# Kernel tuning notes

Hardware: AMD Instinct MI355X
Metric: run time of the kernel (lower is better)

The kernel has to match this reference:

```python
import jax, jax.numpy as jnp
import numpy as np
from jax.scipy.linalg import solve_triangular

S = 64            # number of weight samples (Xi.shape[0])
OUT = 256         # out_channels
IN_CH, K = 64, 3
F = IN_CH * K * K # in_features == inducing_batch == 576
LOG_PREC_INIT = -4.0
LOG_PREC_LR = 1.0


def setup_inputs() -> dict:
    key = jax.random.key(0)
    k1, k2, k3, k4 = jax.random.split(key, 4)
    Xi = jax.random.normal(k1, (S, 128, F), jnp.float32)          # only shape[0] is used
    Xi_param = jax.random.normal(k2, (1, F, F), jnp.float32)      # self.Xi: [1, inducing_batch, in_features]
    u = jax.random.normal(k3, (OUT, F, 1), jnp.float32)           # self.u
    log_prec_scaled = (LOG_PREC_INIT / LOG_PREC_LR) * jnp.ones((1, 1, F), jnp.float32)
    Z = jax.random.normal(k4, (S, OUT, F, 1), jnp.float32)        # internal randn noise, made explicit
    return dict(Xi=Xi, Xi_param=Xi_param, u=u, log_prec_scaled=log_prec_scaled, Z=Z)


def reference(Xi, Xi_param, u, log_prec_scaled, Z):
    S_ = Xi.shape[0]
    Fd = Xi_param.shape[-1]
    O = u.shape[0]
    # log_prec = log_prec_lr * log_prec_scaled  (precs == 1)
    log_prec = LOG_PREC_LR * log_prec_scaled[0]                    # [1, F]
    Xe = jnp.broadcast_to(Xi_param, (S_, Fd, Fd))                  # [S, I, F]
    XiLT = jnp.exp(log_prec) * jnp.swapaxes(Xe, -1, -2)            # [S, F, I]  (prec_L is None branch)
    XiLXi = XiLT @ Xe                                              # [S, F, F]
    XiLY = jnp.einsum('sfi,oi->sfo', XiLT, u[..., 0])              # [S, F, O]  (torch: [S, O, F, 1])
    # NealPrior over in_shape: precision = fan_in * I, fan_in = in_features
    prior_prec = float(Fd)
    prec = XiLXi + prior_prec * jnp.eye(Fd, dtype=XiLXi.dtype)     # [S, F, F]
    L = jnp.linalg.cholesky(prec)
    logdet_prec = 2.0 * jnp.sum(jnp.log(jnp.diagonal(L, axis1=-2, axis2=-1)), -1)  # [S]
    logdet_prec_tot = O * logdet_prec                              # expand(S, O).sum(-1)
    # cholesky_solve(XiLY, L): prec^{-1} XiLY, batched over O via RHS columns
    mean = solve_triangular(L, solve_triangular(L, XiLY, lower=True), lower=True, trans=1)  # [S, F, O]
    Zm = jnp.swapaxes(Z[..., 0], -1, -2)                           # [S, F, O]
    dW = solve_triangular(L, Zm, lower=True, trans=1)              # L^T dW = Z
    sample_fo = mean + dW                                          # [S, F, O]
    sample = jnp.swapaxes(sample_fo, -1, -2)                       # [S, O, F] == self._sample
    # logP = mvnormal_log_prob_unnorm(prior_prec, sample^T):  -0.5 tr(x^T P x) + 0.5*O*logdet(P)
    logP = (-0.5 * prior_prec * jnp.sum(sample_fo ** 2, (-1, -2))
            + 0.5 * O * Fd * jnp.log(jnp.asarray(prior_prec, sample.dtype)))
    logQ = -0.5 * jnp.sum(Z ** 2, (-1, -2, -3)) + 0.5 * logdet_prec_tot
    logpq = logP - logQ                                            # [S]
    return sample, logpq
```

## Files before the change

### kernel.cpp

```cpp
#include <hip/hip_runtime.h>

#define F 576
#define OUTC 256
#define SNUM 64
#define PP 576.0f
#define NBLK 36

__device__ __forceinline__ void gbar(int* cnt, int barid) {
  __syncthreads();
  if (threadIdx.x == 0) {
    __builtin_amdgcn_fence(__ATOMIC_RELEASE, "agent");
    __hip_atomic_fetch_add(cnt, 1, __ATOMIC_RELAXED, __HIP_MEMORY_SCOPE_AGENT);
    int target = barid * NBLK;
    while (__hip_atomic_load(cnt, __ATOMIC_RELAXED, __HIP_MEMORY_SCOPE_AGENT) < target) {
      __builtin_amdgcn_s_sleep(2);
    }
    __builtin_amdgcn_fence(__ATOMIC_ACQUIRE, "agent");
  }
  __syncthreads();
}

__device__ __forceinline__ void mm16(const float (*As)[68], const float (*Bs)[68],
                                     float acc[4][4], int tx, int ty) {
#pragma unroll
  for (int k = 0; k < 32; ++k) {
    float4 a4 = *(const float4*)&As[k][ty * 4];
    float4 b4 = *(const float4*)&Bs[k][tx * 4];
    float av[4] = {a4.x, a4.y, a4.z, a4.w};
    float bv[4] = {b4.x, b4.y, b4.z, b4.w};
#pragma unroll
    for (int r = 0; r < 4; ++r)
#pragma unroll
      for (int c = 0; c < 4; ++c) acc[r][c] += av[r] * bv[c];
  }
}

__device__ void tile_gemm(const float* __restrict__ A, int lda,
                          const float* __restrict__ B, int ldb,
                          float* __restrict__ C, int ldc,
                          int m0, int n0, int K, float sgn,
                          float (*As)[68], float (*Bs)[68]) {
  int t = threadIdx.x, tx = t & 15, ty = t >> 4;
  float acc[4][4] = {};
  for (int k0 = 0; k0 < K; k0 += 32) {
    int rr = t >> 2, kq = t & 3;
    const float* ap = &A[(m0 + rr) * lda + k0 + kq * 8];
    float4 a0 = *(const float4*)ap;
    float4 a1 = *(const float4*)(ap + 4);
    As[kq*8+0][rr] = a0.x; As[kq*8+1][rr] = a0.y;
    As[kq*8+2][rr] = a0.z; As[kq*8+3][rr] = a0.w;
    As[kq*8+4][rr] = a1.x; As[kq*8+5][rr] = a1.y;
    As[kq*8+6][rr] = a1.z; As[kq*8+7][rr] = a1.w;
    int col = t & 63, kr = t >> 6;
#pragma unroll
    for (int kk = 0; kk < 32; kk += 4)
      Bs[kr + kk][col] = B[(k0 + kr + kk) * ldb + n0 + col];
    __syncthreads();
    mm16(As, Bs, acc, tx, ty);
    __syncthreads();
  }
#pragma unroll
  for (int r = 0; r < 4; ++r)
#pragma unroll
    for (int c = 0; c < 4; ++c)
      C[(m0 + ty*4 + r) * ldc + n0 + tx*4 + c] = sgn * acc[r][c];
}

__device__ void diag_factor(float* Ts ) {
  int t = threadIdx.x;
  __syncthreads();
  if (t < 64) {
    int l = t;
    float r[64];
#pragma unroll
    for (int g = 0; g < 64; ++g) r[g] = Ts[l*66 + g];
#pragma unroll
    for (int j = 0; j < 64; ++j) {
      float d = __shfl(r[j], j, 64);
      float inv = 1.0f / sqrtf(d);
      float c = r[j] * inv;
      r[j] = c;
#pragma unroll
      for (int g = j + 1; g < 64; ++g)
        r[g] = fmaf(-__shfl(c, g, 64), c, r[g]);
    }
#pragma unroll
    for (int g = 0; g < 64; ++g) Ts[l*66 + g] = r[g];
  }
  __syncthreads();
}

__device__ void panel_phase(float* __restrict__ G, int k0, int b,
                            float* Ts, float* invd) {
  int t = threadIdx.x;
  for (int idx = t; idx < 64 * 64; idx += 256) {
    int i = idx >> 6, j = idx & 63;
    Ts[i*66 + j] = G[(k0 + i) * F + k0 + j];
  }
  __syncthreads();
  if (t < 64) invd[t] = 1.0f / Ts[t*66 + t];
  __syncthreads();
  int l = t & 63, w = t >> 6;
  int r0 = k0 + 64 + b * 16 + w * 4;
  float v0 = G[(r0 + 0) * F + k0 + l];
  float v1 = G[(r0 + 1) * F + k0 + l];
  float v2 = G[(r0 + 2) * F + k0 + l];
  float v3 = G[(r0 + 3) * F + k0 + l];
#pragma unroll
  for (int j = 0; j < 64; ++j) {
    float dj = invd[j];
    float x0 = __shfl(v0, j, 64) * dj;
    float x1 = __shfl(v1, j, 64) * dj;
    float x2 = __shfl(v2, j, 64) * dj;
    float x3 = __shfl(v3, j, 64) * dj;
    if (l > j) {
      float lj = Ts[l*66 + j];
      v0 = fmaf(-x0, lj, v0);
      v1 = fmaf(-x1, lj, v1);
      v2 = fmaf(-x2, lj, v2);
      v3 = fmaf(-x3, lj, v3);
    }
  }
  float dl = invd[l];
  G[(r0 + 0) * F + k0 + l] = v0 * dl;
  G[(r0 + 1) * F + k0 + l] = v1 * dl;
  G[(r0 + 2) * F + k0 + l] = v2 * dl;
  G[(r0 + 3) * F + k0 + l] = v3 * dl;
}

__device__ void upd_phase(float* __restrict__ G, int k0, int ti, int tj, bool fuse,
                          float (*As)[68], float (*Bs)[68], float* Ts) {
  int b0 = k0 + 64;
  int i0 = b0 + ti * 64, j0 = b0 + tj * 64;
  int t = threadIdx.x, tx = t & 15, ty = t >> 4;
  float acc[4][4] = {};
  for (int kk0 = 0; kk0 < 64; kk0 += 32) {
    for (int idx = t; idx < 64 * 32; idx += 256) {
      int ii = idx >> 5, kk = idx & 31;
      As[kk][ii] = G[(i0 + ii) * F + k0 + kk0 + kk];
      Bs[kk][ii] = G[(j0 + ii) * F + k0 + kk0 + kk];
    }
    __syncthreads();
#pragma unroll
    for (int k = 0; k < 32; ++k) {
      float a[4], b[4];
#pragma unroll
      for (int m = 0; m < 4; ++m) { a[m] = As[k][ty*4 + m]; b[m] = Bs[k][tx*4 + m]; }
#pragma unroll
      for (int r = 0; r < 4; ++r)
#pragma unroll
        for (int c = 0; c < 4; ++c) acc[r][c] += a[r] * b[c];
    }
    __syncthreads();
  }
  if (!fuse) {
#pragma unroll
    for (int r = 0; r < 4; ++r)
#pragma unroll
      for (int c = 0; c < 4; ++c)
        G[(i0 + ty*4 + r) * F + j0 + tx*4 + c] -= acc[r][c];
  } else {
#pragma unroll
    for (int r = 0; r < 4; ++r)
#pragma unroll
      for (int c = 0; c < 4; ++c)
        Ts[(ty*4 + r)*66 + tx*4 + c] =
            G[(i0 + ty*4 + r) * F + j0 + tx*4 + c] - acc[r][c];
    diag_factor(Ts);
    for (int idx = t; idx < 64 * 64; idx += 256) {
      int i = idx >> 6, j = idx & 63;
      if (j <= i) G[(i0 + i) * F + j0 + j] = Ts[i*66 + j];
    }
  }
}

__device__ void base_inv_phase(const float* __restrict__ G, float* __restrict__ LI,
                               int blk, float* Ts, float* invd) {
  int base = blk * 64, t = threadIdx.x;
  for (int idx = t; idx < 64 * 64; idx += 256) {
    int i = idx >> 6, j = idx & 63;
    Ts[i*66 + j] = G[(base + i) * F + base + j];
  }
  __syncthreads();
  if (t < 64) invd[t] = 1.0f / Ts[t*66 + t];
  __syncthreads();
  int l = t & 63, w = t >> 6;
  float v[16];
#pragma unroll
  for (int c = 0; c < 16; ++c) v[c] = (l == (w * 16 + c)) ? 1.0f : 0.0f;
#pragma unroll
  for (int j = 0; j < 64; ++j) {
    float dj = invd[j];
    float lj = (l > j) ? Ts[l*66 + j] : 0.0f;
#pragma unroll
    for (int c = 0; c < 16; ++c) {
      float x = __shfl(v[c], j, 64) * dj;
      v[c] = fmaf(-x, lj, v[c]);
    }
  }
  float dl = invd[l];
#pragma unroll
  for (int c = 0; c < 16; ++c)
    LI[(base + l) * F + base + w * 16 + c] = v[c] * dl;
}

__device__ void mean_phase(const float* __restrict__ LI, const float* __restrict__ T,
                           float* __restrict__ meanT, int bf, int bo,
                           float (*As)[68], float (*Bs)[68]) {
  int t = threadIdx.x, tx = t & 15, ty = t >> 4;
  int f0 = bf * 64, o0 = bo * 64;
  float acc[4][4] = {};
  for (int g0 = f0; g0 < F; g0 += 32) {
    int col = t & 63, kr = t >> 6;
#pragma unroll
    for (int kk = 0; kk < 32; kk += 4) {
      As[kr + kk][col] = T[(g0 + kr + kk) * OUTC + o0 + col];
      Bs[kr + kk][col] = LI[(g0 + kr + kk) * F + f0 + col];
    }
    __syncthreads();
    mm16(As, Bs, acc, tx, ty);
    __syncthreads();
  }
#pragma unroll
  for (int r = 0; r < 4; ++r) {
    float4 st = make_float4(acc[r][0], acc[r][1], acc[r][2], acc[r][3]);
    *(float4*)&meanT[(o0 + ty*4 + r) * F + f0 + tx*4] = st;
  }
}

__global__ __launch_bounds__(256) void k_mid(float* __restrict__ G, float* __restrict__ LI,
                                             const float* __restrict__ Yb,
                                             float* __restrict__ Tb, float* __restrict__ meanT,
                                             int* __restrict__ ctl) {
  __shared__ float As[32][68];
  __shared__ float Bs[32][68];
  __shared__ float Ts[64 * 66];
  __shared__ float invd[64];
  int* cnt = ctl;
  int bar = 0;
  int b = blockIdx.x, t = threadIdx.x;
  float* Tw = Tb;

  if (b == 0) {
    for (int idx = t; idx < 64 * 64; idx += 256) {
      int i = idx >> 6, j = idx & 63;
      Ts[i*66 + j] = G[i * F + j];
    }
    diag_factor(Ts);
    for (int idx = t; idx < 64 * 64; idx += 256) {
      int i = idx >> 6, j = idx & 63;
      if (j <= i) G[i * F + j] = Ts[i*66 + j];
    }
  }
  gbar(cnt, ++bar);

  for (int k = 0; k < 8; ++k) {
    int k0 = k * 64;
    int n = 512 - k0;
    if (b < n / 16) panel_phase(G, k0, b, Ts, invd);
    gbar(cnt, ++bar);
    int nt = n / 64, ntiles = nt * (nt + 1) / 2;
    if (b < ntiles) {
      int ti = 0, bb = b;
      while (bb >= ti + 1) { bb -= ti + 1; ++ti; }
      int tj = bb;
      upd_phase(G, k0, ti, tj, (ti == 0 && tj == 0), As, Bs, Ts);
    }
    gbar(cnt, ++bar);
  }

  if (b < 9) {
    base_inv_phase(G, LI, b, Ts, invd);
  } else {
    int m = b - 9;
    for (int q = m; q < 72; q += 27) {
      int r = q / 8, cc = q % 8;
      int c = cc + (cc >= r ? 1 : 0);
      for (int idx = t; idx < 64 * 16; idx += 256) {
        int i = idx >> 4, jj = idx & 15;
        ((float4*)&LI[(r * 64 + i) * F + c * 64])[jj] = make_float4(0.f, 0.f, 0.f, 0.f);
      }
    }
  }
  gbar(cnt, ++bar);

  if (b < 4) tile_gemm(G + 64*F + b*128*(F+1), F, LI + b*128*(F+1), F,
                       Tw + b*4096, 64, 0, 0, 64, 1.0f, As, Bs);
  gbar(cnt, ++bar);
  if (b < 4) tile_gemm(LI + 64*(F+1) + b*128*(F+1), F, Tw + b*4096, 64,
                       LI + 64*F + b*128*(F+1), F, 0, 0, 64, -1.0f, As, Bs);
  gbar(cnt, ++bar);
  if (b < 8) {
    int z = b >> 2, tl = b & 3;
    tile_gemm(G + 128*F + z*256*(F+1), F, LI + z*256*(F+1), F,
              Tw + z*16384, 128, (tl>>1)*64, (tl&1)*64, 128, 1.0f, As, Bs);
  }
  gbar(cnt, ++bar);
  if (b < 8) {
    int z = b >> 2, tl = b & 3;
    tile_gemm(LI + 128*(F+1) + z*256*(F+1), F, Tw + z*16384, 128,
              LI + 128*F + z*256*(F+1), F, (tl>>1)*64, (tl&1)*64, 128, -1.0f, As, Bs);
  }
  gbar(cnt, ++bar);
  if (b < 16) tile_gemm(G + 256*F, F, LI, F, Tw, 256,
                        (b>>2)*64, (b&3)*64, 256, 1.0f, As, Bs);
  gbar(cnt, ++bar);
  if (b < 16) tile_gemm(LI + 256*(F+1), F, Tw, 256, LI + 256*F, F,
                        (b>>2)*64, (b&3)*64, 256, -1.0f, As, Bs);
  gbar(cnt, ++bar);
  if (b < 8) tile_gemm(G + 512*F, F, LI, F, Tw, 512, 0, b*64, 512, 1.0f, As, Bs);
  gbar(cnt, ++bar);
  if (b < 8) tile_gemm(LI + 512*(F+1), F, Tw, 512, LI + 512*F, F, 0, b*64, 64, -1.0f, As, Bs);
  gbar(cnt, ++bar);

  {
    int bg = b >> 2, bo = b & 3;
    tile_gemm(LI, F, Yb, OUTC, Tb, OUTC, bg * 64, bo * 64, bg * 64 + 64, 1.0f, As, Bs);
  }
  gbar(cnt, ++bar);

  {
    int bf = b >> 2, bo = b & 3;
    mean_phase(LI, Tb, meanT, bf, bo, As, Bs);
  }
}

__global__ __launch_bounds__(256) void k_gy(const float* __restrict__ X,
                                            const float* __restrict__ u,
                                            const float* __restrict__ lp,
                                            float* __restrict__ G,
                                            float* __restrict__ Y) {
  __shared__ float As[32][68];
  __shared__ float Bs[32][68];
  int t = threadIdx.x, tx = t & 15, ty = t >> 4;
  if (blockIdx.z == 0) {
    int bi = blockIdx.y, bj = blockIdx.x;
    if (bj > bi) return;
    int f0 = bi * 64, g0 = bj * 64;
    float acc[4][4] = {};
    for (int i0 = 0; i0 < F; i0 += 32) {
      int col = t & 63, kr = t >> 6;
#pragma unroll
      for (int kk = 0; kk < 32; kk += 4) {
        int i = i0 + kr + kk;
        float e = expf(lp[i]);
        As[kr + kk][col] = e * X[i * F + f0 + col];
        Bs[kr + kk][col] = X[i * F + g0 + col];
      }
      __syncthreads();
      mm16(As, Bs, acc, tx, ty);
      __syncthreads();
    }
#pragma unroll
    for (int r = 0; r < 4; ++r) {
      int gr = f0 + ty*4 + r;
#pragma unroll
      for (int c = 0; c < 4; ++c) {
        int gc = g0 + tx*4 + c;
        float v = acc[r][c];
        if (gr == gc) v += PP;
        G[gr * F + gc] = v;
      }
    }
  } else {
    if (blockIdx.x >= 4) return;
    int bo = blockIdx.x, bf = blockIdx.y;
    int f0 = bf * 64, o0 = bo * 64;
    float acc[4][4] = {};
    for (int i0 = 0; i0 < F; i0 += 32) {
      {
        int col = t & 63, kr = t >> 6;
#pragma unroll
        for (int kk = 0; kk < 32; kk += 4) {
          int i = i0 + kr + kk;
          As[kr + kk][col] = expf(lp[i]) * X[i * F + f0 + col];
        }
        int oo = t >> 2, kq = t & 3;
        const float* ur = &u[(o0 + oo) * F + i0 + kq * 8];
        float4 u0 = *(const float4*)ur;
        float4 u1 = *(const float4*)(ur + 4);
        Bs[kq*8+0][oo] = u0.x; Bs[kq*8+1][oo] = u0.y;
        Bs[kq*8+2][oo] = u0.z; Bs[kq*8+3][oo] = u0.w;
        Bs[kq*8+4][oo] = u1.x; Bs[kq*8+5][oo] = u1.y;
        Bs[kq*8+6][oo] = u1.z; Bs[kq*8+7][oo] = u1.w;
      }
      __syncthreads();
      mm16(As, Bs, acc, tx, ty);
      __syncthreads();
    }
#pragma unroll
    for (int r = 0; r < 4; ++r) {
      float4 st = make_float4(acc[r][0], acc[r][1], acc[r][2], acc[r][3]);
      *(float4*)&Y[(f0 + ty*4 + r) * OUTC + o0 + tx*4] = st;
    }
  }
}

__global__ __launch_bounds__(256) void k_big(const float* __restrict__ Z,
                                             const float* __restrict__ LI,
                                             const float* __restrict__ meanT,
                                             float* __restrict__ out,
                                             double* __restrict__ parts) {
  int bf = blockIdx.x, br = blockIdx.y;
  __shared__ float As[32][68];
  __shared__ float Bs[32][68];
  __shared__ double redA[256];
  __shared__ double redB[256];
  int t = threadIdx.x, tx = t & 15, ty = t >> 4;
  int f0 = bf * 64, r0 = br * 64;
  float acc[4][4] = {};
  double zsq = 0.0;
  for (int g0 = f0; g0 < F; g0 += 32) {
    {
      int rr = t >> 2, kq = t & 3;
      const float* zr = &Z[(r0 + rr) * F + g0 + kq * 8];
      float4 a0 = *(const float4*)zr;
      float4 a1 = *(const float4*)(zr + 4);
      if (bf == 0) {
        zsq += (double)a0.x*a0.x + (double)a0.y*a0.y + (double)a0.z*a0.z + (double)a0.w*a0.w
             + (double)a1.x*a1.x + (double)a1.y*a1.y + (double)a1.z*a1.z + (double)a1.w*a1.w;
      }
      As[kq*8+0][rr] = a0.x; As[kq*8+1][rr] = a0.y;
      As[kq*8+2][rr] = a0.z; As[kq*8+3][rr] = a0.w;
      As[kq*8+4][rr] = a1.x; As[kq*8+5][rr] = a1.y;
      As[kq*8+6][rr] = a1.z; As[kq*8+7][rr] = a1.w;
      int col = t & 63, kr = t >> 6;
#pragma unroll
      for (int kk = 0; kk < 32; kk += 4)
        Bs[kr + kk][col] = LI[(g0 + kr + kk) * F + f0 + col];
    }
    __syncthreads();
    mm16(As, Bs, acc, tx, ty);
    __syncthreads();
  }
  double ssq = 0.0;
#pragma unroll
  for (int r = 0; r < 4; ++r) {
    int row = r0 + ty*4 + r;
    int o = row & 255;
    float4 mv = *(const float4*)&meanT[o * F + f0 + tx*4];
    float4 st = make_float4(acc[r][0] + mv.x, acc[r][1] + mv.y,
                            acc[r][2] + mv.z, acc[r][3] + mv.w);
    *(float4*)&out[row * F + f0 + tx*4] = st;
    ssq += (double)st.x*st.x + (double)st.y*st.y + (double)st.z*st.z + (double)st.w*st.w;
  }
  redA[t] = ssq; redB[t] = zsq;
  __syncthreads();
  for (int o = 128; o > 0; o >>= 1) {
    if (t < o) { redA[t] += redA[t + o]; redB[t] += redB[t + o]; }
    __syncthreads();
  }
  if (t == 0) {
    int s = br >> 2;
    atomicAdd(&parts[s * 2 + 0], redA[0]);
    if (bf == 0) atomicAdd(&parts[s * 2 + 1], redB[0]);
  }
}

__global__ __launch_bounds__(576) void k_logpq_final(const float* __restrict__ LI,
                                                     const double* __restrict__ parts,
                                                     float* __restrict__ out) {
  __shared__ double red[576];
  int t = threadIdx.x;
  red[t] = log((double)LI[t * F + t]);
  __syncthreads();
  for (int o = 512; o > 0; o >>= 1) {
    if (t < o && t + o < 576) red[t] += red[t + o];
    __syncthreads();
  }
  double ldsumLI = red[0];
  if (t < SNUM) {
    double ssq = parts[t * 2 + 0];
    double zsq = parts[t * 2 + 1];
    double pp = 576.0;
    double lpq = -0.5 * pp * ssq
               + 0.5 * (double)(OUTC * F) * log(pp)
               + 0.5 * zsq
               + (double)OUTC * ldsumLI;
    out[SNUM * OUTC * F + t] = (float)lpq;
  }
}

extern "C" void kernel_launch(void* const* d_in, const int* in_sizes, int n_in,
                              void* d_out, int out_size, void* d_ws, size_t ws_size,
                              hipStream_t stream) {
  (void)in_sizes; (void)n_in; (void)out_size; (void)ws_size;
  const float* X  = (const float*)d_in[1];
  const float* u  = (const float*)d_in[2];
  const float* lp = (const float*)d_in[3];
  const float* Z  = (const float*)d_in[4];
  float* out = (float*)d_out;

  float* ws    = (float*)d_ws;
  float* G     = ws;
  float* LI    = ws + 331776;
  float* Yb    = ws + 663552;
  float* Tb    = ws + 811008;
  float* meanT = ws + 958464;
  double* parts = (double*)(ws + 1105920);
  int*    ctl   = (int*)(ws + 1105920 + 256);

  hipMemsetAsync((void*)(ws + 1105920), 0, 1032, stream);
  k_gy<<<dim3(9, 9, 2), 256, 0, stream>>>(X, u, lp, G, Yb);
  k_mid<<<NBLK, 256, 0, stream>>>(G, LI, Yb, Tb, meanT, ctl);
  k_big<<<dim3(9, 256), 256, 0, stream>>>(Z, LI, meanT, out, parts);
  k_logpq_final<<<1, 576, 0, stream>>>(LI, parts, out);
}
```

Baseline: 699.6 us.

## Use split-bf16 MFMA for the big Z·L⁻¹ GEMM and merge barrier phases

The large noise-times-inverse-Cholesky GEMM in k_big now runs on bf16 MFMA instructions instead of FP32 FMAs. Each operand is split into high and low bf16 parts, and three MFMA products are summed to approximate FP32 accuracy. A new k_split kernel transposes L⁻¹ and pre-splits it into bf16 hi/lo arrays, reusing the G workspace. In k_mid, two pairs of dependent tile GEMMs that ran on the same blocks are merged so they share one grid barrier instead of two. The cost is an extra kernel launch and reduced precision compared with a true FP32 GEMM.

```diff
diff --git a/kernel.cpp b/kernel.cpp
--- a/kernel.cpp
+++ b/kernel.cpp
@@ -5,6 +5,16 @@
 #define SNUM 64
 #define PP 576.0f
 #define NBLK 36
+
+typedef unsigned short u16;
+typedef __attribute__((ext_vector_type(8))) short short8;
+typedef __attribute__((ext_vector_type(4))) float f32x4;
+
+__device__ __forceinline__ u16 f2b_rne(float x) {
+  unsigned u = __float_as_uint(x);
+  unsigned r = (u + 0x7FFF + ((u >> 16) & 1)) >> 16;
+  return (u16)r;
+}
 
 __device__ __forceinline__ void gbar(int* cnt, int barid) {
   __syncthreads();
@@ -231,12 +241,11 @@
 __global__ __launch_bounds__(256) void k_mid(float* __restrict__ G, float* __restrict__ LI,
                                              const float* __restrict__ Yb,
                                              float* __restrict__ Tb, float* __restrict__ meanT,
-                                             int* __restrict__ ctl) {
+                                             int* __restrict__ cnt) {
   __shared__ float As[32][68];
   __shared__ float Bs[32][68];
   __shared__ float Ts[64 * 66];
   __shared__ float invd[64];
-  int* cnt = ctl;
   int bar = 0;
   int b = blockIdx.x, t = threadIdx.x;
   float* Tw = Tb;
@@ -284,11 +293,12 @@
   }
   gbar(cnt, ++bar);
 
-  if (b < 4) tile_gemm(G + 64*F + b*128*(F+1), F, LI + b*128*(F+1), F,
-                       Tw + b*4096, 64, 0, 0, 64, 1.0f, As, Bs);
-  gbar(cnt, ++bar);
-  if (b < 4) tile_gemm(LI + 64*(F+1) + b*128*(F+1), F, Tw + b*4096, 64,
-                       LI + 64*F + b*128*(F+1), F, 0, 0, 64, -1.0f, As, Bs);
+  if (b < 4) {
+    tile_gemm(G + 64*F + b*128*(F+1), F, LI + b*128*(F+1), F,
+              Tw + b*4096, 64, 0, 0, 64, 1.0f, As, Bs);
+    tile_gemm(LI + 64*(F+1) + b*128*(F+1), F, Tw + b*4096, 64,
+              LI + 64*F + b*128*(F+1), F, 0, 0, 64, -1.0f, As, Bs);
+  }
   gbar(cnt, ++bar);
   if (b < 8) {
     int z = b >> 2, tl = b & 3;
@@ -308,9 +318,10 @@
   if (b < 16) tile_gemm(LI + 256*(F+1), F, Tw, 256, LI + 256*F, F,
                         (b>>2)*64, (b&3)*64, 256, -1.0f, As, Bs);
   gbar(cnt, ++bar);
-  if (b < 8) tile_gemm(G + 512*F, F, LI, F, Tw, 512, 0, b*64, 512, 1.0f, As, Bs);
-  gbar(cnt, ++bar);
-  if (b < 8) tile_gemm(LI + 512*(F+1), F, Tw, 512, LI + 512*F, F, 0, b*64, 64, -1.0f, As, Bs);
+  if (b < 8) {
+    tile_gemm(G + 512*F, F, LI, F, Tw, 512, 0, b*64, 512, 1.0f, As, Bs);
+    tile_gemm(LI + 512*(F+1), F, Tw, 512, LI + 512*F, F, 0, b*64, 64, -1.0f, As, Bs);
+  }
   gbar(cnt, ++bar);
 
   {
@@ -396,53 +407,127 @@
   }
 }
 
+__global__ __launch_bounds__(256) void k_split(const float* __restrict__ LI,
+                                               u16* __restrict__ H, u16* __restrict__ L) {
+  __shared__ float Tt[64][65];
+  int gb = blockIdx.x, fb = blockIdx.y;
+  int t = threadIdx.x;
+  for (int idx = t; idx < 4096; idx += 256) {
+    int i = idx >> 6, j = idx & 63;
+    Tt[i][j] = LI[(gb * 64 + i) * F + fb * 64 + j];
+  }
+  __syncthreads();
+  for (int idx = t; idx < 4096; idx += 256) {
+    int i = idx >> 6, j = idx & 63;
+    float x = Tt[j][i];
+    u16 h = f2b_rne(x);
+    float hf = __uint_as_float((unsigned)h << 16);
+    H[(fb * 64 + i) * F + gb * 64 + j] = h;
+    L[(fb * 64 + i) * F + gb * 64 + j] = f2b_rne(x - hf);
+  }
+}
+
+#define PADK 72
 __global__ __launch_bounds__(256) void k_big(const float* __restrict__ Z,
-                                             const float* __restrict__ LI,
+                                             const u16* __restrict__ BHg,
+                                             const u16* __restrict__ BLg,
                                              const float* __restrict__ meanT,
                                              float* __restrict__ out,
                                              double* __restrict__ parts) {
   int bf = blockIdx.x, br = blockIdx.y;
-  __shared__ float As[32][68];
-  __shared__ float Bs[32][68];
+  __shared__ u16 ZH[64 * PADK];
+  __shared__ u16 ZL[64 * PADK];
+  __shared__ u16 BH[64 * PADK];
+  __shared__ u16 BL[64 * PADK];
   __shared__ double redA[256];
   __shared__ double redB[256];
-  int t = threadIdx.x, tx = t & 15, ty = t >> 4;
+  int t = threadIdx.x, l = t & 63, w = t >> 6;
   int f0 = bf * 64, r0 = br * 64;
-  float acc[4][4] = {};
+  int rr = t >> 2, kq = t & 3;
+  f32x4 acc0 = {0.f,0.f,0.f,0.f}, acc1 = {0.f,0.f,0.f,0.f};
+  f32x4 acc2 = {0.f,0.f,0.f,0.f}, acc3 = {0.f,0.f,0.f,0.f};
   double zsq = 0.0;
-  for (int g0 = f0; g0 < F; g0 += 32) {
+
+  for (int g0 = f0; g0 < F; g0 += 64) {
     {
-      int rr = t >> 2, kq = t & 3;
-      const float* zr = &Z[(r0 + rr) * F + g0 + kq * 8];
-      float4 a0 = *(const float4*)zr;
-      float4 a1 = *(const float4*)(zr + 4);
-      if (bf == 0) {
-        zsq += (double)a0.x*a0.x + (double)a0.y*a0.y + (double)a0.z*a0.z + (double)a0.w*a0.w
-             + (double)a1.x*a1.x + (double)a1.y*a1.y + (double)a1.z*a1.z + (double)a1.w*a1.w;
-      }
-      As[kq*8+0][rr] = a0.x; As[kq*8+1][rr] = a0.y;
-      As[kq*8+2][rr] = a0.z; As[kq*8+3][rr] = a0.w;
-      As[kq*8+4][rr] = a1.x; As[kq*8+5][rr] = a1.y;
-      As[kq*8+6][rr] = a1.z; As[kq*8+7][rr] = a1.w;
-      int col = t & 63, kr = t >> 6;
-#pragma unroll
-      for (int kk = 0; kk < 32; kk += 4)
-        Bs[kr + kk][col] = LI[(g0 + kr + kk) * F + f0 + col];
-    }
-    __syncthreads();
-    mm16(As, Bs, acc, tx, ty);
-    __syncthreads();
-  }
+      const float* zp = &Z[(r0 + rr) * F + g0 + kq * 16];
+      float xs[16];
+      *(float4*)&xs[0]  = *(const float4*)(zp + 0);
+      *(float4*)&xs[4]  = *(const float4*)(zp + 4);
+      *(float4*)&xs[8]  = *(const float4*)(zp + 8);
+      *(float4*)&xs[12] = *(const float4*)(zp + 12);
+      u16 hh[16], ll[16];
+#pragma unroll
+      for (int j = 0; j < 16; ++j) {
+        u16 h = f2b_rne(xs[j]);
+        float hf = __uint_as_float((unsigned)h << 16);
+        hh[j] = h;
+        ll[j] = f2b_rne(xs[j] - hf);
+        if (bf == 0) zsq += (double)xs[j] * xs[j];
+      }
+      *(short8*)&ZH[rr * PADK + kq * 16 + 0] = *(short8*)&hh[0];
+      *(short8*)&ZH[rr * PADK + kq * 16 + 8] = *(short8*)&hh[8];
+      *(short8*)&ZL[rr * PADK + kq * 16 + 0] = *(short8*)&ll[0];
+      *(short8*)&ZL[rr * PADK + kq * 16 + 8] = *(short8*)&ll[8];
+      const u16* bh = &BHg[(f0 + rr) * F + g0 + kq * 16];
+      const u16* bl = &BLg[(f0 + rr) * F + g0 + kq * 16];
+      *(short8*)&BH[rr * PADK + kq * 16 + 0] = *(const short8*)(bh + 0);
+      *(short8*)&BH[rr * PADK + kq * 16 + 8] = *(const short8*)(bh + 8);
+      *(short8*)&BL[rr * PADK + kq * 16 + 0] = *(const short8*)(bl + 0);
+      *(short8*)&BL[rr * PADK + kq * 16 + 8] = *(const short8*)(bl + 8);
+    }
+    __syncthreads();
+#pragma unroll
+    for (int kk = 0; kk < 2; ++kk) {
+      int aoff = (w * 16 + (l & 15)) * PADK + kk * 32 + (l >> 4) * 8;
+      short8 ah = *(short8*)&ZH[aoff];
+      short8 al = *(short8*)&ZL[aoff];
+      int b0o = ((l & 15)) * PADK + kk * 32 + (l >> 4) * 8;
+      {
+        short8 bh = *(short8*)&BH[b0o];
+        short8 bl = *(short8*)&BL[b0o];
+        acc0 = __builtin_amdgcn_mfma_f32_16x16x32_bf16(ah, bh, acc0, 0, 0, 0);
+        acc0 = __builtin_amdgcn_mfma_f32_16x16x32_bf16(ah, bl, acc0, 0, 0, 0);
+        acc0 = __builtin_amdgcn_mfma_f32_16x16x32_bf16(al, bh, acc0, 0, 0, 0);
+      }
+      {
+        short8 bh = *(short8*)&BH[b0o + 16 * PADK];
+        short8 bl = *(short8*)&BL[b0o + 16 * PADK];
+        acc1 = __builtin_amdgcn_mfma_f32_16x16x32_bf16(ah, bh, acc1, 0, 0, 0);
+        acc1 = __builtin_amdgcn_mfma_f32_16x16x32_bf16(ah, bl, acc1, 0, 0, 0);
+        acc1 = __builtin_amdgcn_mfma_f32_16x16x32_bf16(al, bh, acc1, 0, 0, 0);
+      }
+      {
+        short8 bh = *(short8*)&BH[b0o + 32 * PADK];
+        short8 bl = *(short8*)&BL[b0o + 32 * PADK];
+        acc2 = __builtin_amdgcn_mfma_f32_16x16x32_bf16(ah, bh, acc2, 0, 0, 0);
+        acc2 = __builtin_amdgcn_mfma_f32_16x16x32_bf16(ah, bl, acc2, 0, 0, 0);
+        acc2 = __builtin_amdgcn_mfma_f32_16x16x32_bf16(al, bh, acc2, 0, 0, 0);
+      }
+      {
+        short8 bh = *(short8*)&BH[b0o + 48 * PADK];
+        short8 bl = *(short8*)&BL[b0o + 48 * PADK];
+        acc3 = __builtin_amdgcn_mfma_f32_16x16x32_bf16(ah, bh, acc3, 0, 0, 0);
+        acc3 = __builtin_amdgcn_mfma_f32_16x16x32_bf16(ah, bl, acc3, 0, 0, 0);
+        acc3 = __builtin_amdgcn_mfma_f32_16x16x32_bf16(al, bh, acc3, 0, 0, 0);
+      }
+    }
+    __syncthreads();
+  }
+
   double ssq = 0.0;
-#pragma unroll
-  for (int r = 0; r < 4; ++r) {
-    int row = r0 + ty*4 + r;
-    int o = row & 255;
-    float4 mv = *(const float4*)&meanT[o * F + f0 + tx*4];
-    float4 st = make_float4(acc[r][0] + mv.x, acc[r][1] + mv.y,
-                            acc[r][2] + mv.z, acc[r][3] + mv.w);
-    *(float4*)&out[row * F + f0 + tx*4] = st;
-    ssq += (double)st.x*st.x + (double)st.y*st.y + (double)st.z*st.z + (double)st.w*st.w;
+  int colb = l & 15, rq = l >> 4;
+#pragma unroll
+  for (int c = 0; c < 4; ++c) {
+    f32x4 a = (c == 0) ? acc0 : (c == 1) ? acc1 : (c == 2) ? acc2 : acc3;
+#pragma unroll
+    for (int r = 0; r < 4; ++r) {
+      int row = r0 + w * 16 + rq * 4 + r;
+      int col = f0 + c * 16 + colb;
+      float v = a[r] + meanT[(row & 255) * F + col];
+      out[row * F + col] = v;
+      ssq += (double)v * v;
+    }
   }
   redA[t] = ssq; redB[t] = zsq;
   __syncthreads();
@@ -498,11 +583,14 @@
   float* Tb    = ws + 811008;
   float* meanT = ws + 958464;
   double* parts = (double*)(ws + 1105920);
-  int*    ctl   = (int*)(ws + 1105920 + 256);
+  int*    cnt   = (int*)(ws + 1105920 + 256);
+  u16* LIT_H = (u16*)G;
+  u16* LIT_L = LIT_H + 331776;
 
   hipMemsetAsync((void*)(ws + 1105920), 0, 1032, stream);
   k_gy<<<dim3(9, 9, 2), 256, 0, stream>>>(X, u, lp, G, Yb);
-  k_mid<<<NBLK, 256, 0, stream>>>(G, LI, Yb, Tb, meanT, ctl);
-  k_big<<<dim3(9, 256), 256, 0, stream>>>(Z, LI, meanT, out, parts);
+  k_mid<<<NBLK, 256, 0, stream>>>(G, LI, Yb, Tb, meanT, cnt);
+  k_split<<<dim3(9, 9), 256, 0, stream>>>(LI, LIT_H, LIT_L);
+  k_big<<<dim3(9, 256), 256, 0, stream>>>(Z, LIT_H, LIT_L, meanT, out, parts);
   k_logpq_final<<<1, 576, 0, stream>>>(LI, parts, out);
 }
```

New measurement: 651.3 us. 6.9% less time.
